# Kernel tuning notes

Hardware: AMD Instinct MI355X
Metric: run time of the kernel (lower is better)

The kernel has to match this reference:

```python
import jax, jax.numpy as jnp
import numpy as np

BETA = 1.0
EPS = 1e-12  # F.normalize eps

def _normalize(x):
    # F.normalize(x, dim=1): x shape (B, N, 1)
    n = jnp.sqrt(jnp.sum(x * x, axis=1, keepdims=True))
    return x / jnp.maximum(n, EPS)

def _step(M, x):
    return _normalize(jnp.matmul(M, x))

def _eigval(M, x):
    # x^T M x / ||x||^2, x: (B, N, 1)
    Mx = jnp.matmul(M, x)                          # (B, N, 1)
    num = jnp.sum(Mx * x, axis=(1, 2))             # (B,)
    den = jnp.sum(x * x, axis=(1, 2))              # (B,)
    return num / den

def setup_inputs() -> dict:
    key = jax.random.key(0)
    kA, kx = jax.random.split(key)
    A = jax.random.normal(kA, (64, 512, 28, 28), dtype=jnp.float32)
    x0 = jax.random.normal(kx, (64, 512, 1), dtype=jnp.float32)
    return {"A": A, "x0": x0}

def reference(A, x0):
    B, C, H, W = A.shape
    Wm = A.reshape(B, C, H * W)                    # (B, C, HW)
    AAT = jnp.einsum('bcd,bed->bce', Wm, Wm)       # (B, C, C)

    # --- dominant_eigenvalue(AAT): first call initializes last_x (no grad, 3 iters) ---
    xi = _normalize(x0)
    for _ in range(3):
        xi = _step(AAT, xi)
    xi = jax.lax.stop_gradient(xi)                 # last_x after no-grad init
    x1 = _step(AAT, xi)                            # 1 differentiable iter
    largest = _eigval(AAT, x1)                     # (B,)
    last_x = jax.lax.stop_gradient(x1)             # self.last_x = x.detach()

    # --- dominant_eigenvalue(AAT - largest*I): reuses last_x, 1 iter ---
    I = jnp.eye(C, dtype=A.dtype)[None]            # (1, C, C)
    A2 = AAT - largest[:, None, None] * I
    x2 = _step(A2, last_x)
    tmp = _eigval(A2, x2)

    smallest = tmp + largest
    penalty = BETA * (largest / smallest - 1.0) ** 2
    return jnp.sum(penalty) / B
```

## Files before the change

kernel.cpp:

```cpp
#include <hip/hip_runtime.h>
#include <math.h>


#define BB 64
#define CC 512
#define DD 784
#define DCH 16
#define NSPLIT 7
#define NCHPS 7
#define F4PR 196
#define BF4 100352
#define FEPS 1e-12f

typedef float f4v __attribute__((ext_vector_type(4)));

__device__ __forceinline__ void gload16(const float4* gp, float4* lp) {
    __builtin_amdgcn_global_load_lds(
        (const __attribute__((address_space(1))) void*)gp,
        (__attribute__((address_space(3))) void*)lp, 16, 0, 0);
}

__device__ __forceinline__ float blk_reduce(float s, float* red) {
    for (int off = 32; off; off >>= 1) s += __shfl_down(s, off, 64);
    int w = threadIdx.x >> 6;
    if ((threadIdx.x & 63) == 0) red[w] = s;
    __syncthreads();
    float t = red[0] + red[1] + red[2] + red[3];
    __syncthreads();
    return t;
}

__global__ __launch_bounds__(256, 3)
void k_repack(const float* __restrict__ A, float* __restrict__ T) {
    __shared__ float4 lds4[16 * F4PR];
    const int tid = threadIdx.x, lane = tid & 63, w = tid >> 6;
    const int b = blockIdx.y, c0 = blockIdx.x * 16;
    const float4* src4 = (const float4*)A + ((size_t)b * CC + c0) * F4PR;
#pragma unroll
    for (int i = 0; i < 12; i++)
        gload16(src4 + i * 256 + w * 64 + lane, lds4 + i * 256 + w * 64);
    if (w == 0) gload16(src4 + 3072 + lane, lds4 + 3072);
    __syncthreads();
    float4* dst4 = (float4*)T + (size_t)b * BF4;
#pragma unroll
    for (int j = 0; j < 13; j++) {
        int idx = j * 256 + tid;
        if (idx < 3136) {
            int chq = idx >> 4, i = idx & 15;
            dst4[(size_t)chq * CC + c0 + i] = lds4[i * F4PR + chq];
        }
    }
}

template <bool RP>
__global__ __launch_bounds__(256, 2)
void k_step(const float* __restrict__ M, const float* __restrict__ xin,
            const int nparts, float* __restrict__ vout) {
    __shared__ float xs[CC];
    __shared__ float vws[4][CC];
    __shared__ float red[4];

    const int tid = threadIdx.x;
    const int b = blockIdx.y, s = blockIdx.x;
    const int lane = tid & 63, w = tid >> 6;
    const float4* Mb = (const float4*)M + (size_t)b * BF4;

    const float* xp = xin + (size_t)b * nparts * CC;
    float xv0 = 0.f, xv1 = 0.f;
    for (int p = 0; p < nparts; p++) {
        xv0 += xp[p * CC + tid];
        xv1 += xp[p * CC + tid + 256];
    }
    float ss = blk_reduce(xv0 * xv0 + xv1 * xv1, red);
    float rn = 1.0f / fmaxf(sqrtf(ss), FEPS);
    xs[tid] = xv0 * rn;
    xs[tid + 256] = xv1 * rn;
    __syncthreads();

    float xk[8];
#pragma unroll
    for (int k = 0; k < 8; k++) xk[k] = xs[lane + 64 * k];

    const int ch0 = s * NCHPS;
    f4v a[2][8];
    float vk[8] = {0.f, 0.f, 0.f, 0.f, 0.f, 0.f, 0.f, 0.f};

    auto load = [&](int ch, f4v* dst) {
        if (RP) {
            const f4v* g = (const f4v*)(Mb + (size_t)(ch * 4 + w) * CC + lane);
#pragma unroll
            for (int k = 0; k < 8; k++)
                dst[k] = __builtin_nontemporal_load(g + 64 * k);
        } else {
            const f4v* g = (const f4v*)(Mb + (size_t)lane * F4PR + ch * 4 + w);
#pragma unroll
            for (int k = 0; k < 8; k++) dst[k] = g[(size_t)64 * k * F4PR];
        }
    };

    load(ch0, a[0]);
#pragma unroll
    for (int j = 0; j < NCHPS; j++) {
        const int cb = j & 1;
        if (j + 1 < NCHPS) load(ch0 + j + 1, a[cb ^ 1]);

        f4v ua = {0.f, 0.f, 0.f, 0.f};
#pragma unroll
        for (int k = 0; k < 8; k++) {
            ua.x += a[cb][k].x * xk[k]; ua.y += a[cb][k].y * xk[k];
            ua.z += a[cb][k].z * xk[k]; ua.w += a[cb][k].w * xk[k];
        }
#pragma unroll
        for (int off = 1; off < 64; off <<= 1) {
            ua.x += __shfl_xor(ua.x, off, 64);
            ua.y += __shfl_xor(ua.y, off, 64);
            ua.z += __shfl_xor(ua.z, off, 64);
            ua.w += __shfl_xor(ua.w, off, 64);
        }

#pragma unroll
        for (int k = 0; k < 8; k++)
            vk[k] += a[cb][k].x * ua.x + a[cb][k].y * ua.y +
                     a[cb][k].z * ua.z + a[cb][k].w * ua.w;
    }

#pragma unroll
    for (int k = 0; k < 8; k++) vws[w][lane + 64 * k] = vk[k];
    __syncthreads();
    float* vp = vout + ((size_t)b * NSPLIT + s) * CC;
    vp[tid]       = vws[0][tid] + vws[1][tid] + vws[2][tid] + vws[3][tid];
    vp[tid + 256] = vws[0][tid + 256] + vws[1][tid + 256] +
                    vws[2][tid + 256] + vws[3][tid + 256];
}

__global__ void k_mid(const float* __restrict__ t4, const float* __restrict__ t5,
                      float* __restrict__ acc, float* __restrict__ y) {
    __shared__ float red[4];
    int b = blockIdx.x;
    const float* p4 = t4 + (size_t)b * NSPLIT * CC;
    const float* p5 = t5 + (size_t)b * NSPLIT * CC;
    float a0 = 0.f, a1 = 0.f, b0 = 0.f, b1 = 0.f;
    for (int p = 0; p < NSPLIT; p++) {
        a0 += p4[p * CC + threadIdx.x]; a1 += p4[p * CC + threadIdx.x + 256];
        b0 += p5[p * CC + threadIdx.x]; b1 += p5[p * CC + threadIdx.x + 256];
    }
    float ss4 = blk_reduce(a0 * a0 + a1 * a1, red);
    float rn = 1.0f / fmaxf(sqrtf(ss4), FEPS);
    float x10 = a0 * rn, x11 = a1 * rn;
    float num = blk_reduce(b0 * x10 + b1 * x11, red);
    float den = blk_reduce(x10 * x10 + x11 * x11, red);
    float largest = num / den;
    float* yp = y + (size_t)b * CC;
    yp[threadIdx.x] = b0 - largest * x10;
    yp[threadIdx.x + 256] = b1 - largest * x11;
    if (threadIdx.x == 0) acc[b * 8 + 0] = largest;
}

__global__ void k_fin2(const float* __restrict__ w, const float* __restrict__ y,
                       float* __restrict__ acc) {
    __shared__ float red[4];
    int b = blockIdx.x;
    const float* wp = w + (size_t)b * NSPLIT * CC;
    const float* yp = y + (size_t)b * CC;
    float w0 = 0.f, w1 = 0.f;
    for (int p = 0; p < NSPLIT; p++) {
        w0 += wp[p * CC + threadIdx.x];
        w1 += wp[p * CC + threadIdx.x + 256];
    }
    float y0 = yp[threadIdx.x], y1 = yp[threadIdx.x + 256];
    float ssy = blk_reduce(y0 * y0 + y1 * y1, red);
    float rn = 1.0f / fmaxf(sqrtf(ssy), FEPS);
    float x20 = y0 * rn, x21 = y1 * rn;
    float dotwx = blk_reduce(w0 * x20 + w1 * x21, red);
    float den2 = blk_reduce(x20 * x20 + x21 * x21, red);
    if (threadIdx.x == 0) { acc[b * 8 + 1] = dotwx; acc[b * 8 + 2] = den2; }
}

__global__ void k_out(const float* __restrict__ acc, float* __restrict__ out) {
    int b = threadIdx.x;
    float largest = acc[b * 8 + 0];
    float dotwx   = acc[b * 8 + 1];
    float den2    = acc[b * 8 + 2];
    float tmp = (dotwx - largest * den2) / den2;
    float smallest = tmp + largest;
    float r = largest / smallest - 1.0f;
    float pen = r * r;
    for (int off = 32; off; off >>= 1) pen += __shfl_down(pen, off, 64);
    if (b == 0) out[0] = pen / (float)BB;
}

extern "C" void kernel_launch(void* const* d_in, const int* in_sizes, int n_in,
                              void* d_out, int out_size, void* d_ws, size_t ws_size,
                              hipStream_t stream) {
    const float* A  = (const float*)d_in[0];
    const float* x0 = (const float*)d_in[1];
    float* out = (float*)d_out;
    float* ws = (float*)d_ws;

    float* acc = ws;
    float* Y   = ws + 512;
    float* PA  = Y + BB * CC;
    float* PB  = PA + (size_t)BB * NSPLIT * CC;
    float* T   = PB + (size_t)BB * NSPLIT * CC;
    const size_t need =
        ((size_t)512 + BB * CC + 2 * (size_t)BB * NSPLIT * CC +
         (size_t)BB * CC * DD) * sizeof(float);

    dim3 gS(NSPLIT, BB);
    if (ws_size >= need) {
        k_repack<<<dim3(32, BB), 256, 0, stream>>>(A, T);
        k_step<true><<<gS, 256, 0, stream>>>(T, x0, 1, PA);
        k_step<true><<<gS, 256, 0, stream>>>(T, PA, NSPLIT, PB);
        k_step<true><<<gS, 256, 0, stream>>>(T, PB, NSPLIT, PA);
        k_step<true><<<gS, 256, 0, stream>>>(T, PA, NSPLIT, PB);
        k_step<true><<<gS, 256, 0, stream>>>(T, PB, NSPLIT, PA);
        k_mid<<<BB, 256, 0, stream>>>(PB, PA, acc, Y);
        k_step<true><<<gS, 256, 0, stream>>>(T, Y, 1, PB);
        k_fin2<<<BB, 256, 0, stream>>>(PB, Y, acc);
    } else {
        k_step<false><<<gS, 256, 0, stream>>>(A, x0, 1, PA);
        k_step<false><<<gS, 256, 0, stream>>>(A, PA, NSPLIT, PB);
        k_step<false><<<gS, 256, 0, stream>>>(A, PB, NSPLIT, PA);
        k_step<false><<<gS, 256, 0, stream>>>(A, PA, NSPLIT, PB);
        k_step<false><<<gS, 256, 0, stream>>>(A, PB, NSPLIT, PA);
        k_mid<<<BB, 256, 0, stream>>>(PB, PA, acc, Y);
        k_step<false><<<gS, 256, 0, stream>>>(A, Y, 1, PB);
        k_fin2<<<BB, 256, 0, stream>>>(PB, Y, acc);
    }
    k_out<<<1, 64, 0, stream>>>(acc, out);
}
```

Baseline: 283.8 us.

## Split step kernel into eight parts and prefetch matrix before normalization

The step kernel now uses eight splits of six chunks each, with the last split handling one extra chunk, so the 49 chunks cover a larger grid. The first two chunk loads are issued before the input-vector reduction and normalization, hiding that latency behind them. The nontemporal hint on the matrix loads is dropped, which may let the repacked matrix stay in cache across repeated steps. The uneven work in the last split and more partial vectors for the reducers add some imbalance and overhead.

```diff
diff --git a/kernel.cpp b/kernel.cpp
--- a/kernel.cpp
+++ b/kernel.cpp
@@ -5,9 +5,7 @@
 #define BB 64
 #define CC 512
 #define DD 784
-#define DCH 16
-#define NSPLIT 7
-#define NCHPS 7
+#define NSPLIT 8
 #define F4PR 196
 #define BF4 100352
 #define FEPS 1e-12f
@@ -65,6 +63,47 @@
     const int lane = tid & 63, w = tid >> 6;
     const float4* Mb = (const float4*)M + (size_t)b * BF4;
 
+    float xk[8];
+    float vk[8] = {0.f, 0.f, 0.f, 0.f, 0.f, 0.f, 0.f, 0.f};
+
+    auto load = [&](int ch, f4v* dst) {
+        if (RP) {
+            const f4v* g = (const f4v*)(Mb + (size_t)(ch * 4 + w) * CC + lane);
+#pragma unroll
+            for (int k = 0; k < 8; k++) dst[k] = g[64 * k];
+        } else {
+            const f4v* g = (const f4v*)(Mb + (size_t)lane * F4PR + ch * 4 + w);
+#pragma unroll
+            for (int k = 0; k < 8; k++) dst[k] = g[(size_t)64 * k * F4PR];
+        }
+    };
+    auto computeq = [&](const f4v* a) {
+        f4v ua = {0.f, 0.f, 0.f, 0.f};
+#pragma unroll
+        for (int k = 0; k < 8; k++) {
+            ua.x += a[k].x * xk[k]; ua.y += a[k].y * xk[k];
+            ua.z += a[k].z * xk[k]; ua.w += a[k].w * xk[k];
+        }
+#pragma unroll
+        for (int off = 1; off < 64; off <<= 1) {
+            ua.x += __shfl_xor(ua.x, off, 64);
+            ua.y += __shfl_xor(ua.y, off, 64);
+            ua.z += __shfl_xor(ua.z, off, 64);
+            ua.w += __shfl_xor(ua.w, off, 64);
+        }
+#pragma unroll
+        for (int k = 0; k < 8; k++)
+            vk[k] += a[k].x * ua.x + a[k].y * ua.y +
+                     a[k].z * ua.z + a[k].w * ua.w;
+    };
+
+    const int ch0 = s * 6;
+    const bool x7 = (s == NSPLIT - 1);
+
+    f4v ra[8], rb[8];
+    load(ch0, ra);
+    load(ch0 + 1, rb);
+
     const float* xp = xin + (size_t)b * nparts * CC;
     float xv0 = 0.f, xv1 = 0.f;
     for (int p = 0; p < nparts; p++) {
@@ -76,53 +115,17 @@
     xs[tid] = xv0 * rn;
     xs[tid + 256] = xv1 * rn;
     __syncthreads();
-
-    float xk[8];
 #pragma unroll
     for (int k = 0; k < 8; k++) xk[k] = xs[lane + 64 * k];
 
-    const int ch0 = s * NCHPS;
-    f4v a[2][8];
-    float vk[8] = {0.f, 0.f, 0.f, 0.f, 0.f, 0.f, 0.f, 0.f};
-
-    auto load = [&](int ch, f4v* dst) {
-        if (RP) {
-            const f4v* g = (const f4v*)(Mb + (size_t)(ch * 4 + w) * CC + lane);
-#pragma unroll
-            for (int k = 0; k < 8; k++)
-                dst[k] = __builtin_nontemporal_load(g + 64 * k);
-        } else {
-            const f4v* g = (const f4v*)(Mb + (size_t)lane * F4PR + ch * 4 + w);
-#pragma unroll
-            for (int k = 0; k < 8; k++) dst[k] = g[(size_t)64 * k * F4PR];
-        }
-    };
-
-    load(ch0, a[0]);
-#pragma unroll
-    for (int j = 0; j < NCHPS; j++) {
-        const int cb = j & 1;
-        if (j + 1 < NCHPS) load(ch0 + j + 1, a[cb ^ 1]);
-
-        f4v ua = {0.f, 0.f, 0.f, 0.f};
-#pragma unroll
-        for (int k = 0; k < 8; k++) {
-            ua.x += a[cb][k].x * xk[k]; ua.y += a[cb][k].y * xk[k];
-            ua.z += a[cb][k].z * xk[k]; ua.w += a[cb][k].w * xk[k];
-        }
-#pragma unroll
-        for (int off = 1; off < 64; off <<= 1) {
-            ua.x += __shfl_xor(ua.x, off, 64);
-            ua.y += __shfl_xor(ua.y, off, 64);
-            ua.z += __shfl_xor(ua.z, off, 64);
-            ua.w += __shfl_xor(ua.w, off, 64);
-        }
-
-#pragma unroll
-        for (int k = 0; k < 8; k++)
-            vk[k] += a[cb][k].x * ua.x + a[cb][k].y * ua.y +
-                     a[cb][k].z * ua.z + a[cb][k].w * ua.w;
-    }
+    computeq(ra); load(ch0 + 2, ra);
+    computeq(rb); load(ch0 + 3, rb);
+    computeq(ra); load(ch0 + 4, ra);
+    computeq(rb); load(ch0 + 5, rb);
+    computeq(ra);
+    if (x7) load(48, ra);
+    computeq(rb);
+    if (x7) computeq(ra);
 
 #pragma unroll
     for (int k = 0; k < 8; k++) vws[w][lane + 64 * k] = vk[k];
```

Result: slower. 335.0 us (+18.1%).

## Fuse the repack of A into the first power-iteration step kernel

Applied to the files above, without the earlier changes.

Removes the separate repack kernel and instead has the first power-iteration step read A in its original layout and write the repacked tile to T as it streams through it. This saves one full read of A (about 100 MB) and a kernel launch. The cost is that the first step uses the strided original-layout loads. The later steps also drop the nontemporal loads and switch from ext_vector_type to plain float4, which may change cache behaviour.

```diff
diff --git a/kernel.cpp b/kernel.cpp
--- a/kernel.cpp
+++ b/kernel.cpp
@@ -5,21 +5,12 @@
 #define BB 64
 #define CC 512
 #define DD 784
-#define DCH 16
 #define NSPLIT 7
 #define NCHPS 7
 #define F4PR 196
 #define BF4 100352
 #define FEPS 1e-12f
 
-typedef float f4v __attribute__((ext_vector_type(4)));
-
-__device__ __forceinline__ void gload16(const float4* gp, float4* lp) {
-    __builtin_amdgcn_global_load_lds(
-        (const __attribute__((address_space(1))) void*)gp,
-        (__attribute__((address_space(3))) void*)lp, 16, 0, 0);
-}
-
 __device__ __forceinline__ float blk_reduce(float s, float* red) {
     for (int off = 32; off; off >>= 1) s += __shfl_down(s, off, 64);
     int w = threadIdx.x >> 6;
@@ -30,26 +21,80 @@
     return t;
 }
 
-__global__ __launch_bounds__(256, 3)
-void k_repack(const float* __restrict__ A, float* __restrict__ T) {
-    __shared__ float4 lds4[16 * F4PR];
-    const int tid = threadIdx.x, lane = tid & 63, w = tid >> 6;
-    const int b = blockIdx.y, c0 = blockIdx.x * 16;
-    const float4* src4 = (const float4*)A + ((size_t)b * CC + c0) * F4PR;
-#pragma unroll
-    for (int i = 0; i < 12; i++)
-        gload16(src4 + i * 256 + w * 64 + lane, lds4 + i * 256 + w * 64);
-    if (w == 0) gload16(src4 + 3072 + lane, lds4 + 3072);
-    __syncthreads();
-    float4* dst4 = (float4*)T + (size_t)b * BF4;
-#pragma unroll
-    for (int j = 0; j < 13; j++) {
-        int idx = j * 256 + tid;
-        if (idx < 3136) {
-            int chq = idx >> 4, i = idx & 15;
-            dst4[(size_t)chq * CC + c0 + i] = lds4[i * F4PR + chq];
-        }
-    }
+__global__ __launch_bounds__(256, 2)
+void k_step1f(const float* __restrict__ A, const float* __restrict__ xin,
+              float* __restrict__ T, float* __restrict__ vout) {
+    __shared__ float xs[CC];
+    __shared__ float vws[4][CC];
+    __shared__ float red[4];
+
+    const int tid = threadIdx.x;
+    const int b = blockIdx.y, s = blockIdx.x;
+    const int lane = tid & 63, w = tid >> 6;
+    const float4* Ab = (const float4*)A + (size_t)b * BF4;
+    float4* Tb = (float4*)T + (size_t)b * BF4;
+
+    const float* xp = xin + (size_t)b * CC;
+    float xv0 = xp[tid], xv1 = xp[tid + 256];
+    float ss = blk_reduce(xv0 * xv0 + xv1 * xv1, red);
+    float rn = 1.0f / fmaxf(sqrtf(ss), FEPS);
+    xs[tid] = xv0 * rn;
+    xs[tid + 256] = xv1 * rn;
+    __syncthreads();
+
+    float xk[8];
+#pragma unroll
+    for (int k = 0; k < 8; k++) xk[k] = xs[lane + 64 * k];
+
+    const int ch0 = s * NCHPS;
+    float4 a[2][8];
+    float vk[8] = {0.f, 0.f, 0.f, 0.f, 0.f, 0.f, 0.f, 0.f};
+
+    auto load = [&](int ch, float4* dst) {
+        const float4* g = Ab + (size_t)lane * F4PR + ch * 4 + w;
+#pragma unroll
+        for (int k = 0; k < 8; k++) dst[k] = g[(size_t)64 * k * F4PR];
+    };
+
+    load(ch0, a[0]);
+#pragma unroll
+    for (int j = 0; j < NCHPS; j++) {
+        const int cb = j & 1;
+        if (j + 1 < NCHPS) load(ch0 + j + 1, a[cb ^ 1]);
+
+        {
+            float4* d = Tb + (size_t)((ch0 + j) * 4 + w) * CC + lane;
+#pragma unroll
+            for (int k = 0; k < 8; k++) d[64 * k] = a[cb][k];
+        }
+
+        float4 ua = make_float4(0.f, 0.f, 0.f, 0.f);
+#pragma unroll
+        for (int k = 0; k < 8; k++) {
+            ua.x += a[cb][k].x * xk[k]; ua.y += a[cb][k].y * xk[k];
+            ua.z += a[cb][k].z * xk[k]; ua.w += a[cb][k].w * xk[k];
+        }
+#pragma unroll
+        for (int off = 1; off < 64; off <<= 1) {
+            ua.x += __shfl_xor(ua.x, off, 64);
+            ua.y += __shfl_xor(ua.y, off, 64);
+            ua.z += __shfl_xor(ua.z, off, 64);
+            ua.w += __shfl_xor(ua.w, off, 64);
+        }
+
+#pragma unroll
+        for (int k = 0; k < 8; k++)
+            vk[k] += a[cb][k].x * ua.x + a[cb][k].y * ua.y +
+                     a[cb][k].z * ua.z + a[cb][k].w * ua.w;
+    }
+
+#pragma unroll
+    for (int k = 0; k < 8; k++) vws[w][lane + 64 * k] = vk[k];
+    __syncthreads();
+    float* vp = vout + ((size_t)b * NSPLIT + s) * CC;
+    vp[tid]       = vws[0][tid] + vws[1][tid] + vws[2][tid] + vws[3][tid];
+    vp[tid + 256] = vws[0][tid + 256] + vws[1][tid + 256] +
+                    vws[2][tid + 256] + vws[3][tid + 256];
 }
 
 template <bool RP>
@@ -82,17 +127,16 @@
     for (int k = 0; k < 8; k++) xk[k] = xs[lane + 64 * k];
 
     const int ch0 = s * NCHPS;
-    f4v a[2][8];
+    float4 a[2][8];
     float vk[8] = {0.f, 0.f, 0.f, 0.f, 0.f, 0.f, 0.f, 0.f};
 
-    auto load = [&](int ch, f4v* dst) {
+    auto load = [&](int ch, float4* dst) {
         if (RP) {
-            const f4v* g = (const f4v*)(Mb + (size_t)(ch * 4 + w) * CC + lane);
-#pragma unroll
-            for (int k = 0; k < 8; k++)
-                dst[k] = __builtin_nontemporal_load(g + 64 * k);
+            const float4* g = Mb + (size_t)(ch * 4 + w) * CC + lane;
+#pragma unroll
+            for (int k = 0; k < 8; k++) dst[k] = g[64 * k];
         } else {
-            const f4v* g = (const f4v*)(Mb + (size_t)lane * F4PR + ch * 4 + w);
+            const float4* g = Mb + (size_t)lane * F4PR + ch * 4 + w;
 #pragma unroll
             for (int k = 0; k < 8; k++) dst[k] = g[(size_t)64 * k * F4PR];
         }
@@ -104,7 +148,7 @@
         const int cb = j & 1;
         if (j + 1 < NCHPS) load(ch0 + j + 1, a[cb ^ 1]);
 
-        f4v ua = {0.f, 0.f, 0.f, 0.f};
+        float4 ua = make_float4(0.f, 0.f, 0.f, 0.f);
 #pragma unroll
         for (int k = 0; k < 8; k++) {
             ua.x += a[cb][k].x * xk[k]; ua.y += a[cb][k].y * xk[k];
@@ -208,8 +252,7 @@
 
     dim3 gS(NSPLIT, BB);
     if (ws_size >= need) {
-        k_repack<<<dim3(32, BB), 256, 0, stream>>>(A, T);
-        k_step<true><<<gS, 256, 0, stream>>>(T, x0, 1, PA);
+        k_step1f<<<gS, 256, 0, stream>>>(A, x0, T, PA);
         k_step<true><<<gS, 256, 0, stream>>>(T, PA, NSPLIT, PB);
         k_step<true><<<gS, 256, 0, stream>>>(T, PB, NSPLIT, PA);
         k_step<true><<<gS, 256, 0, stream>>>(T, PA, NSPLIT, PB);
```

New measurement: 275.2 us. 3.0% less time.
